# Kernel optimization log

Hardware: AMD Instinct MI355X
Metric: run time of the kernel (lower is better)

Reference implementation:

```python
import jax, jax.numpy as jnp
import numpy as np

B, T, M, L_TP = 32, 4096, 256, 128


def setup_inputs() -> dict:
    key = jax.random.key(0)
    k1, k2, k3, k4 = jax.random.split(key, 4)
    h_1 = jax.random.normal(k1, (B, T, M), dtype=jnp.float32)
    h_2 = jax.random.normal(k2, (B, T, M), dtype=jnp.float32)
    # trunc_normal(mean=-0.1, std=0.1) approximated by clipped normal
    w_tp = jnp.clip(-0.1 + 0.1 * jax.random.normal(k3, (1, L_TP), dtype=jnp.float32), -0.3, 0.1)
    v_tp = jnp.clip(-0.1 + 0.1 * jax.random.normal(k4, (L_TP, M), dtype=jnp.float32), -0.3, 0.1)
    return {"h_1": h_1, "h_2": h_2, "w_tp": w_tp, "v_tp": v_tp}


def reference(h_1, h_2, w_tp, v_tp):
    # Batched over all T timesteps at once (original loops in Python).
    # h: (B, T, 2, M) -- the 2-way stack of the two streams per timestep
    h = jnp.stack([h_1, h_2], axis=2)
    # tanh MLP hidden: (B, T, 2, L_tp)
    temp = jnp.tanh(jnp.einsum('lm,btcm->btcl', v_tp, h))
    # attention logits: (B, T, 2); softmax over the 2-way axis
    scores = jnp.einsum('l,btcl->btc', w_tp[0], temp)
    A = jax.nn.softmax(scores, axis=2)
    # original returns permute of concat (T, 2, B) -> (B, 2, T)
    return jnp.transpose(A, (0, 2, 1))
```

## Files before the change

### kernel.cpp

```cpp
#include <hip/hip_runtime.h>


typedef unsigned short u16;
typedef unsigned int   u32;
typedef __bf16 bf16x8 __attribute__((ext_vector_type(8)));
typedef float  f32x4  __attribute__((ext_vector_type(4)));

union ABFrag { bf16x8 v; u16 u[8]; uint4 q4; };

__device__ __forceinline__ u16 f2bf(float f) {
  u32 u = __float_as_uint(f);
  u += 0x7fffu + ((u >> 16) & 1u);
  return (u16)(u >> 16);
}

__device__ __forceinline__ float fast_tanh(float x) {
  float t = __builtin_amdgcn_exp2f(2.885390082f * x);
  return 1.0f - 2.0f * __builtin_amdgcn_rcpf(t + 1.0f);
}

typedef const __attribute__((address_space(1))) void gvoid;
typedef __attribute__((address_space(3))) void lvoid;

__device__ __forceinline__ void dma16(const char* g, char* l) {
  __builtin_amdgcn_global_load_lds((gvoid*)g, (lvoid*)l, 16, 0, 0);
}

#define NWG    256
#define ITERS  8
#define TOT    (ITERS * 8)
#define ITSTR  (NWG * 64 * 1024)
#define SMEMSZ (65536 + 8 * 3 * 2048)

__global__ __launch_bounds__(512, 2) void topo_attn_kernel(
    const float* __restrict__ h1, const float* __restrict__ h2,
    const float* __restrict__ w,  const float* __restrict__ vfp,
    float* __restrict__ out) {
  extern __shared__ __align__(16) char smem[];
  u16*  vlds   = (u16*)smem;
  char* albase = smem + 65536;

  const int tid = threadIdx.x;

  {
    const float4* src = (const float4*)vfp;
    #pragma unroll
    for (int k = 0; k < 8; ++k) {
      int gi = k * 512 + tid;
      float4 f0 = src[gi * 2];
      float4 f1 = src[gi * 2 + 1];
      ABFrag t;
      t.u[0] = f2bf(f0.x); t.u[1] = f2bf(f0.y); t.u[2] = f2bf(f0.z); t.u[3] = f2bf(f0.w);
      t.u[4] = f2bf(f1.x); t.u[5] = f2bf(f1.y); t.u[6] = f2bf(f1.z); t.u[7] = f2bf(f1.w);
      int l = gi >> 5;
      int g = gi & 31;
      *(uint4*)&vlds[(l << 8) + (((g + l) & 31) << 3)] = t.q4;
    }
  }
  __syncthreads();

  const int lane = tid & 63;
  const int wave = tid >> 6;
  const int l15  = lane & 15;
  const int q    = lane >> 4;

  float wreg[8];
  #pragma unroll
  for (int lt = 0; lt < 8; ++lt) wreg[lt] = w[lt * 16 + l15];

  char* aslot = albase + wave * 6144;

  const int rr = lane >> 3;
  const int cc = lane & 7;
  const int gchunk = (cc - rr) & 7;

  const int n0base = (blockIdx.x * 8 + wave) * 8;
  const char* g1 = (const char*)h1 + (size_t)(n0base + rr) * 1024 + gchunk * 16;
  const char* g2 = (const char*)h2 + (size_t)(n0base + rr) * 1024 + gchunk * 16;

  const int r7 = l15 & 7;
  const int fragbase = (l15 >> 3) * 1024 + r7 * 128;
  const int j1 = ((2 * q + r7) & 7) * 16;
  const int j2 = ((2 * q + 1 + r7) & 7) * 16;

  {
    dma16(g1, aslot);            dma16(g2, aslot + 1024);
    dma16(g1 + 128, aslot + 2048); dma16(g2 + 128, aslot + 2048 + 1024);
  }

  #pragma unroll
  for (int it = 0; it < ITERS; ++it) {
    f32x4 acc[8];
    #pragma unroll
    for (int lt = 0; lt < 8; ++lt) acc[lt] = (f32x4){0.f, 0.f, 0.f, 0.f};

    #pragma unroll
    for (int ks = 0; ks < 8; ++ks) {
      const int s = it * 8 + ks;
      if (s + 2 < TOT) {
        const int s2 = s + 2;
        const size_t off = (size_t)(s2 >> 3) * ITSTR + (s2 & 7) * 128;
        char* dst = aslot + (s2 % 3) * 2048;
        dma16(g1 + off, dst);
        dma16(g2 + off, dst + 1024);
      }
      if (s + 2 < TOT)      asm volatile("s_waitcnt vmcnt(4)" ::: "memory");
      else if (s + 1 < TOT) asm volatile("s_waitcnt vmcnt(2)" ::: "memory");
      else                  asm volatile("s_waitcnt vmcnt(0)" ::: "memory");

      const char* ab = aslot + (s % 3) * 2048 + fragbase;
      float4 fa = *(const float4*)(ab + j1);
      float4 fb = *(const float4*)(ab + j2);
      ABFrag a;
      a.u[0] = f2bf(fa.x); a.u[1] = f2bf(fa.y); a.u[2] = f2bf(fa.z); a.u[3] = f2bf(fa.w);
      a.u[4] = f2bf(fb.x); a.u[5] = f2bf(fb.y); a.u[6] = f2bf(fb.z); a.u[7] = f2bf(fb.w);
      #pragma unroll
      for (int lt = 0; lt < 8; ++lt) {
        const int l = (lt << 4) + l15;
        bf16x8 bfr = *(const bf16x8*)&vlds[(l << 8) + (((4 * ks + q + l) & 31) << 3)];
        acc[lt] = __builtin_amdgcn_mfma_f32_16x16x32_bf16(a.v, bfr, acc[lt], 0, 0, 0);
      }
    }

    float s_p[4] = {0.f, 0.f, 0.f, 0.f};
    #pragma unroll
    for (int lt = 0; lt < 8; ++lt) {
      #pragma unroll
      for (int r = 0; r < 4; ++r)
        s_p[r] += wreg[lt] * fast_tanh(acc[lt][r]);
    }
    #pragma unroll
    for (int r = 0; r < 4; ++r) {
      #pragma unroll
      for (int off = 1; off < 16; off <<= 1)
        s_p[r] += __shfl_xor(s_p[r], off);
    }
    const int r = l15 & 3;
    float sel = (r == 0) ? s_p[0] : (r == 1) ? s_p[1] : (r == 2) ? s_p[2] : s_p[3];
    float oth = __shfl_xor(sel, 32);
    if (q < 2 && l15 < 4) {
      int n = n0base + it * (NWG * 64) + q * 4 + l15;
      int b = n >> 12, t = n & 4095;
      float e  = __builtin_amdgcn_exp2f(-1.442695041f * (sel - oth));
      float a0 = __builtin_amdgcn_rcpf(1.0f + e);
      out[b * 8192 + t]        = a0;
      out[b * 8192 + 4096 + t] = 1.0f - a0;
    }
  }
}

extern "C" void kernel_launch(void* const* d_in, const int* in_sizes, int n_in,
                              void* d_out, int out_size, void* d_ws, size_t ws_size,
                              hipStream_t stream) {
  const float* h1 = (const float*)d_in[0];
  const float* h2 = (const float*)d_in[1];
  const float* w  = (const float*)d_in[2];
  const float* v  = (const float*)d_in[3];
  float* out = (float*)d_out;

  static int attr_set = 0;
  (void)attr_set;
  hipFuncSetAttribute((const void*)topo_attn_kernel,
                      hipFuncAttributeMaxDynamicSharedMemorySize, SMEMSZ);
  topo_attn_kernel<<<NWG, 512, SMEMSZ, stream>>>(h1, h2, w, v, out);
}
```

Measured before the change: 278.5 us.

## Load activations directly into registers instead of LDS DMA ring buffer

Replaces the per-wave triple-buffered global_load_lds staging of h1/h2 with direct float4 register loads, software-pipelined two steps ahead. Without that staging area LDS use falls to 64KB, and the grid doubles to 512 workgroups with half the iterations each, with launch bounds raised to 4 waves per SIMD for occupancy. This removes the LDS round trip and explicit vmcnt waits. The cost is higher register pressure under the tighter launch bounds, and each lane now issues two 16-byte loads with a stride between rows.

```diff
diff --git a/kernel.cpp b/kernel.cpp
--- a/kernel.cpp
+++ b/kernel.cpp
@@ -19,26 +19,18 @@
   return 1.0f - 2.0f * __builtin_amdgcn_rcpf(t + 1.0f);
 }
 
-typedef const __attribute__((address_space(1))) void gvoid;
-typedef __attribute__((address_space(3))) void lvoid;
+#define NWG    512
+#define ITERS  4
+#define TOT    (ITERS * 8)
+#define ROWS_PER_IT (NWG * 64)
+#define SMEMSZ 65536
 
-__device__ __forceinline__ void dma16(const char* g, char* l) {
-  __builtin_amdgcn_global_load_lds((gvoid*)g, (lvoid*)l, 16, 0, 0);
-}
-
-#define NWG    256
-#define ITERS  8
-#define TOT    (ITERS * 8)
-#define ITSTR  (NWG * 64 * 1024)
-#define SMEMSZ (65536 + 8 * 3 * 2048)
-
-__global__ __launch_bounds__(512, 2) void topo_attn_kernel(
+__global__ __launch_bounds__(512, 4) void topo_attn_kernel(
     const float* __restrict__ h1, const float* __restrict__ h2,
     const float* __restrict__ w,  const float* __restrict__ vfp,
     float* __restrict__ out) {
   extern __shared__ __align__(16) char smem[];
-  u16*  vlds   = (u16*)smem;
-  char* albase = smem + 65536;
+  u16* vlds = (u16*)smem;
 
   const int tid = threadIdx.x;
 
@@ -68,25 +60,21 @@
   #pragma unroll
   for (int lt = 0; lt < 8; ++lt) wreg[lt] = w[lt * 16 + l15];
 
-  char* aslot = albase + wave * 6144;
+  const int n0base = (blockIdx.x * 8 + wave) * 8;
 
-  const int rr = lane >> 3;
-  const int cc = lane & 7;
-  const int gchunk = (cc - rr) & 7;
+  const float* ap = (l15 < 8)
+      ? h1 + (size_t)(n0base + l15) * 256
+      : h2 + (size_t)(n0base + l15 - 8) * 256;
+  ap += q * 8;
 
-  const int n0base = (blockIdx.x * 8 + wave) * 8;
-  const char* g1 = (const char*)h1 + (size_t)(n0base + rr) * 1024 + gchunk * 16;
-  const char* g2 = (const char*)h2 + (size_t)(n0base + rr) * 1024 + gchunk * 16;
+  #define LDA(s, x, y) do {                                                       \
+    const float* _p = ap + (size_t)((s) >> 3) * ((size_t)ROWS_PER_IT * 256)       \
+                         + ((s) & 7) * 32;                                        \
+    (x) = *(const float4*)_p; (y) = *(const float4*)(_p + 4); } while (0)
 
-  const int r7 = l15 & 7;
-  const int fragbase = (l15 >> 3) * 1024 + r7 * 128;
-  const int j1 = ((2 * q + r7) & 7) * 16;
-  const int j2 = ((2 * q + 1 + r7) & 7) * 16;
-
-  {
-    dma16(g1, aslot);            dma16(g2, aslot + 1024);
-    dma16(g1 + 128, aslot + 2048); dma16(g2 + 128, aslot + 2048 + 1024);
-  }
+  float4 cfa, cfb, nfa, nfb;
+  LDA(0, cfa, cfb);
+  LDA(1, nfa, nfb);
 
   #pragma unroll
   for (int it = 0; it < ITERS; ++it) {
@@ -97,29 +85,20 @@
     #pragma unroll
     for (int ks = 0; ks < 8; ++ks) {
       const int s = it * 8 + ks;
-      if (s + 2 < TOT) {
-        const int s2 = s + 2;
-        const size_t off = (size_t)(s2 >> 3) * ITSTR + (s2 & 7) * 128;
-        char* dst = aslot + (s2 % 3) * 2048;
-        dma16(g1 + off, dst);
-        dma16(g2 + off, dst + 1024);
-      }
-      if (s + 2 < TOT)      asm volatile("s_waitcnt vmcnt(4)" ::: "memory");
-      else if (s + 1 < TOT) asm volatile("s_waitcnt vmcnt(2)" ::: "memory");
-      else                  asm volatile("s_waitcnt vmcnt(0)" ::: "memory");
+      float4 mfa = cfa, mfb = cfb;
+      if (s + 2 < TOT) LDA(s + 2, mfa, mfb);
 
-      const char* ab = aslot + (s % 3) * 2048 + fragbase;
-      float4 fa = *(const float4*)(ab + j1);
-      float4 fb = *(const float4*)(ab + j2);
       ABFrag a;
-      a.u[0] = f2bf(fa.x); a.u[1] = f2bf(fa.y); a.u[2] = f2bf(fa.z); a.u[3] = f2bf(fa.w);
-      a.u[4] = f2bf(fb.x); a.u[5] = f2bf(fb.y); a.u[6] = f2bf(fb.z); a.u[7] = f2bf(fb.w);
+      a.u[0] = f2bf(cfa.x); a.u[1] = f2bf(cfa.y); a.u[2] = f2bf(cfa.z); a.u[3] = f2bf(cfa.w);
+      a.u[4] = f2bf(cfb.x); a.u[5] = f2bf(cfb.y); a.u[6] = f2bf(cfb.z); a.u[7] = f2bf(cfb.w);
+
       #pragma unroll
       for (int lt = 0; lt < 8; ++lt) {
         const int l = (lt << 4) + l15;
         bf16x8 bfr = *(const bf16x8*)&vlds[(l << 8) + (((4 * ks + q + l) & 31) << 3)];
         acc[lt] = __builtin_amdgcn_mfma_f32_16x16x32_bf16(a.v, bfr, acc[lt], 0, 0, 0);
       }
+      cfa = nfa; cfb = nfb; nfa = mfa; nfb = mfb;
     }
 
     float s_p[4] = {0.f, 0.f, 0.f, 0.f};
@@ -139,7 +118,7 @@
     float sel = (r == 0) ? s_p[0] : (r == 1) ? s_p[1] : (r == 2) ? s_p[2] : s_p[3];
     float oth = __shfl_xor(sel, 32);
     if (q < 2 && l15 < 4) {
-      int n = n0base + it * (NWG * 64) + q * 4 + l15;
+      int n = n0base + it * ROWS_PER_IT + q * 4 + l15;
       int b = n >> 12, t = n & 4095;
       float e  = __builtin_amdgcn_exp2f(-1.442695041f * (sel - oth));
       float a0 = __builtin_amdgcn_rcpf(1.0f + e);
@@ -158,8 +137,6 @@
   const float* v  = (const float*)d_in[3];
   float* out = (float*)d_out;
 
-  static int attr_set = 0;
-  (void)attr_set;
   hipFuncSetAttribute((const void*)topo_attn_kernel,
                       hipFuncAttributeMaxDynamicSharedMemorySize, SMEMSZ);
   topo_attn_kernel<<<NWG, 512, SMEMSZ, stream>>>(h1, h2, w, v, out);
```

Result: slower. 294.7 us (+5.8%).

## Process two 16-row MFMA tiles per wave to reuse weight fragments

Applied to the files above, without the earlier changes.

Each wave now handles 16 rows (two MFMA tiles) per iteration instead of 8, with half as many outer iterations. Every weight fragment read from LDS feeds two MFMAs, which halves LDS traffic for v per unit of work and doubles the bytes in flight per pipeline stage. The cost is more accumulator registers and twice the per-wave LDS staging space. Shared memory grows to about 160KB per block, which may reduce occupancy under the 2-blocks launch bound.

```diff
diff --git a/kernel.cpp b/kernel.cpp
--- a/kernel.cpp
+++ b/kernel.cpp
@@ -27,10 +27,11 @@
 }
 
 #define NWG    256
-#define ITERS  8
+#define ITERS  4
 #define TOT    (ITERS * 8)
-#define ITSTR  (NWG * 64 * 1024)
-#define SMEMSZ (65536 + 8 * 3 * 2048)
+#define ROWS_PER_IT (NWG * 8 * 16)
+#define ITSTR  ((size_t)ROWS_PER_IT * 1024)
+#define SMEMSZ (65536 + 8 * 3 * 4096)
 
 __global__ __launch_bounds__(512, 2) void topo_attn_kernel(
     const float* __restrict__ h1, const float* __restrict__ h2,
@@ -68,13 +69,13 @@
   #pragma unroll
   for (int lt = 0; lt < 8; ++lt) wreg[lt] = w[lt * 16 + l15];
 
-  char* aslot = albase + wave * 6144;
+  char* aslot = albase + wave * 12288;
 
   const int rr = lane >> 3;
   const int cc = lane & 7;
   const int gchunk = (cc - rr) & 7;
 
-  const int n0base = (blockIdx.x * 8 + wave) * 8;
+  const int n0base = (blockIdx.x * 8 + wave) * 16;
   const char* g1 = (const char*)h1 + (size_t)(n0base + rr) * 1024 + gchunk * 16;
   const char* g2 = (const char*)h2 + (size_t)(n0base + rr) * 1024 + gchunk * 16;
 
@@ -83,68 +84,84 @@
   const int j1 = ((2 * q + r7) & 7) * 16;
   const int j2 = ((2 * q + 1 + r7) & 7) * 16;
 
-  {
-    dma16(g1, aslot);            dma16(g2, aslot + 1024);
-    dma16(g1 + 128, aslot + 2048); dma16(g2 + 128, aslot + 2048 + 1024);
-  }
+  #define STAGE(s) do {                                                          \
+    const size_t off = (size_t)((s) >> 3) * ITSTR + ((s) & 7) * 128;             \
+    char* d = aslot + ((s) % 3) * 4096;                                          \
+    dma16(g1 + off,        d);        dma16(g2 + off,        d + 1024);          \
+    dma16(g1 + off + 8192, d + 2048); dma16(g2 + off + 8192, d + 3072);          \
+  } while (0)
+
+  STAGE(0);
+  STAGE(1);
 
   #pragma unroll
   for (int it = 0; it < ITERS; ++it) {
-    f32x4 acc[8];
+    f32x4 acc0[8], acc1[8];
     #pragma unroll
-    for (int lt = 0; lt < 8; ++lt) acc[lt] = (f32x4){0.f, 0.f, 0.f, 0.f};
+    for (int lt = 0; lt < 8; ++lt) {
+      acc0[lt] = (f32x4){0.f, 0.f, 0.f, 0.f};
+      acc1[lt] = (f32x4){0.f, 0.f, 0.f, 0.f};
+    }
 
     #pragma unroll
     for (int ks = 0; ks < 8; ++ks) {
       const int s = it * 8 + ks;
       if (s + 2 < TOT) {
-        const int s2 = s + 2;
-        const size_t off = (size_t)(s2 >> 3) * ITSTR + (s2 & 7) * 128;
-        char* dst = aslot + (s2 % 3) * 2048;
-        dma16(g1 + off, dst);
-        dma16(g2 + off, dst + 1024);
+        STAGE(s + 2);
+        asm volatile("s_waitcnt vmcnt(8)" ::: "memory");
+      } else if (s + 1 < TOT) {
+        asm volatile("s_waitcnt vmcnt(4)" ::: "memory");
+      } else {
+        asm volatile("s_waitcnt vmcnt(0)" ::: "memory");
       }
-      if (s + 2 < TOT)      asm volatile("s_waitcnt vmcnt(4)" ::: "memory");
-      else if (s + 1 < TOT) asm volatile("s_waitcnt vmcnt(2)" ::: "memory");
-      else                  asm volatile("s_waitcnt vmcnt(0)" ::: "memory");
 
-      const char* ab = aslot + (s % 3) * 2048 + fragbase;
+      const char* ab = aslot + (s % 3) * 4096 + fragbase;
       float4 fa = *(const float4*)(ab + j1);
       float4 fb = *(const float4*)(ab + j2);
-      ABFrag a;
-      a.u[0] = f2bf(fa.x); a.u[1] = f2bf(fa.y); a.u[2] = f2bf(fa.z); a.u[3] = f2bf(fa.w);
-      a.u[4] = f2bf(fb.x); a.u[5] = f2bf(fb.y); a.u[6] = f2bf(fb.z); a.u[7] = f2bf(fb.w);
+      float4 ga = *(const float4*)(ab + 2048 + j1);
+      float4 gb = *(const float4*)(ab + 2048 + j2);
+      ABFrag a0, a1;
+      a0.u[0] = f2bf(fa.x); a0.u[1] = f2bf(fa.y); a0.u[2] = f2bf(fa.z); a0.u[3] = f2bf(fa.w);
+      a0.u[4] = f2bf(fb.x); a0.u[5] = f2bf(fb.y); a0.u[6] = f2bf(fb.z); a0.u[7] = f2bf(fb.w);
+      a1.u[0] = f2bf(ga.x); a1.u[1] = f2bf(ga.y); a1.u[2] = f2bf(ga.z); a1.u[3] = f2bf(ga.w);
+      a1.u[4] = f2bf(gb.x); a1.u[5] = f2bf(gb.y); a1.u[6] = f2bf(gb.z); a1.u[7] = f2bf(gb.w);
+
       #pragma unroll
       for (int lt = 0; lt < 8; ++lt) {
         const int l = (lt << 4) + l15;
         bf16x8 bfr = *(const bf16x8*)&vlds[(l << 8) + (((4 * ks + q + l) & 31) << 3)];
-        acc[lt] = __builtin_amdgcn_mfma_f32_16x16x32_bf16(a.v, bfr, acc[lt], 0, 0, 0);
+        acc0[lt] = __builtin_amdgcn_mfma_f32_16x16x32_bf16(a0.v, bfr, acc0[lt], 0, 0, 0);
+        acc1[lt] = __builtin_amdgcn_mfma_f32_16x16x32_bf16(a1.v, bfr, acc1[lt], 0, 0, 0);
       }
     }
 
-    float s_p[4] = {0.f, 0.f, 0.f, 0.f};
     #pragma unroll
-    for (int lt = 0; lt < 8; ++lt) {
+    for (int tile = 0; tile < 2; ++tile) {
+      const f32x4* acc = tile ? acc1 : acc0;
+      float s_p[4] = {0.f, 0.f, 0.f, 0.f};
       #pragma unroll
-      for (int r = 0; r < 4; ++r)
-        s_p[r] += wreg[lt] * fast_tanh(acc[lt][r]);
-    }
-    #pragma unroll
-    for (int r = 0; r < 4; ++r) {
+      for (int lt = 0; lt < 8; ++lt) {
+        #pragma unroll
+        for (int r = 0; r < 4; ++r)
+          s_p[r] += wreg[lt] * fast_tanh(acc[lt][r]);
+      }
       #pragma unroll
-      for (int off = 1; off < 16; off <<= 1)
-        s_p[r] += __shfl_xor(s_p[r], off);
-    }
-    const int r = l15 & 3;
-    float sel = (r == 0) ? s_p[0] : (r == 1) ? s_p[1] : (r == 2) ? s_p[2] : s_p[3];
-    float oth = __shfl_xor(sel, 32);
-    if (q < 2 && l15 < 4) {
-      int n = n0base + it * (NWG * 64) + q * 4 + l15;
-      int b = n >> 12, t = n & 4095;
-      float e  = __builtin_amdgcn_exp2f(-1.442695041f * (sel - oth));
-      float a0 = __builtin_amdgcn_rcpf(1.0f + e);
-      out[b * 8192 + t]        = a0;
-      out[b * 8192 + 4096 + t] = 1.0f - a0;
+      for (int r = 0; r < 4; ++r) {
+        #pragma unroll
+        for (int off = 1; off < 16; off <<= 1)
+          s_p[r] += __shfl_xor(s_p[r], off);
+      }
+      const int r = l15 & 3;
+      float sel = (r == 0) ? s_p[0] : (r == 1) ? s_p[1] : (r == 2) ? s_p[2] : s_p[3];
+      float oth = __shfl_xor(sel, 32);
+      if (q < 2 && l15 < 4) {
+        int n = n0base + it * ROWS_PER_IT + tile * 8 + q * 4 + l15;
+        int b = n >> 12, t = n & 4095;
+        float e  = __builtin_amdgcn_exp2f(-1.442695041f * (sel - oth));
+        float a0v = __builtin_amdgcn_rcpf(1.0f + e);
+        out[b * 8192 + t]        = a0v;
+        out[b * 8192 + 4096 + t] = 1.0f - a0v;
+      }
     }
   }
 }
@@ -158,8 +175,6 @@
   const float* v  = (const float*)d_in[3];
   float* out = (float*)d_out;
 
-  static int attr_set = 0;
-  (void)attr_set;
   hipFuncSetAttribute((const void*)topo_attn_kernel,
                       hipFuncAttributeMaxDynamicSharedMemorySize, SMEMSZ);
   topo_attn_kernel<<<NWG, 512, SMEMSZ, stream>>>(h1, h2, w, v, out);
```

After: 288.4 us. 1.04x slower.
